# Kernel tuning notes

Measured on AMD Instinct MI355X. Metric: run time of the kernel, lower is better.

Reference implementation:

```python
import jax, jax.numpy as jnp
import numpy as np

N_ATOMS = 100000
N_EDGES = 6400000
CUTOFF = 12.0
CUTOFF_SR = 2.0
CUTOFF_SQ = CUTOFF * CUTOFF
KEHALF = 7.199822675975274  # ASE kehalf, unit factors = 1


def poly6_switch(d, cutoff):
    # Poly6 smooth switch-off: 1 at d=0, 0 at d>=cutoff
    x = d / cutoff
    sw = 1.0 - 10.0 * x**3 + 15.0 * x**4 - 6.0 * x**5
    return jnp.where(d < cutoff, sw, jnp.zeros_like(sw))


def setup_inputs() -> dict:
    key = jax.random.key(0)
    k1, k2, k3, k4, k5 = jax.random.split(key, 5)
    atomic_charges = jax.random.normal(k1, (N_ATOMS,), dtype=jnp.float32) * 0.3
    atomic_dipoles = jax.random.normal(k2, (N_ATOMS,), dtype=jnp.float32) * 0.1
    # distances in (0.5, 13.5): some pairs inside short-range, some beyond cutoff
    distances = jax.random.uniform(k3, (N_EDGES,), dtype=jnp.float32) * 13.0 + 0.5
    idx_i = jax.random.randint(k4, (N_EDGES,), 0, N_ATOMS, dtype=jnp.int32)
    idx_j = jax.random.randint(k5, (N_EDGES,), 0, N_ATOMS, dtype=jnp.int32)
    return {
        "atomic_charges": atomic_charges,
        "atomic_dipoles": atomic_dipoles,
        "distances": distances,
        "idx_i": idx_i,
        "idx_j": idx_j,
    }


def reference(atomic_charges, atomic_dipoles, distances, idx_i, idx_j):
    # gather per-edge charges / dipoles
    qi = atomic_charges[idx_i]
    qj = atomic_charges[idx_j]
    di = atomic_dipoles[idx_i]
    dj = atomic_dipoles[idx_j]

    d = distances
    d_sh = jnp.sqrt(d * d + 1.0)  # shielded distance

    sw_off = poly6_switch(d, CUTOFF_SR)
    sw_on = 1.0 - sw_off

    # split_distance=True branch (cutoff != cutoff_short_range):
    # shifted-force Coulomb (charge-charge, ~1/d)
    E_ord_q = 1.0 / d + d / CUTOFF_SQ - 2.0 / CUTOFF
    E_sh_q = 1.0 / d_sh + d_sh / CUTOFF_SQ - 2.0 / CUTOFF
    E_q = KEHALF * qi * qj * (sw_off * E_sh_q + sw_on * E_ord_q)

    # dipole-dipole term (~1/d^3), same shielded/ordinary blending
    E_ord_d = 1.0 / d**3
    E_sh_d = 1.0 / d_sh**3
    E_d = KEHALF * di * dj * (sw_off * E_sh_d + sw_on * E_ord_d)

    E = E_q + E_d
    E = jnp.where(d <= CUTOFF, E, jnp.zeros_like(E))

    # scatter-sum per-edge energies to atoms
    return jax.ops.segment_sum(E, idx_i, num_segments=N_ATOMS)
```

## Files before the change

kernel.cpp:

```cpp
#include <hip/hip_runtime.h>
#include <hip/hip_bf16.h>
#include <hip/hip_fp16.h>

#define CUTOFF_C    12.0f
#define CUTOFF_SR_C 2.0f
#define CUTOFF_SQ_C 144.0f
#define KEHALF_C    7.199822675975274f

#define BLK1   1024

#define CH_DUO   17408
#define LUT_DUO  1024
#define CH_SOLO  33792
#define LUT_SOLO 2048

#define CH_REC   20000

__device__ __forceinline__ float edge_energy(float d, float qi, float qj,
                                             float di, float dj) {
    float inv_d   = __frcp_rn(d);
    float dsh     = __fsqrt_rn(fmaf(d, d, 1.0f));
    float inv_dsh = __frcp_rn(dsh);
    float x  = d * (1.0f / CUTOFF_SR_C);
    float x3 = x * x * x;
    float sw = fmaf(x3, fmaf(x, fmaf(x, -6.0f, 15.0f), -10.0f), 1.0f);
    float sw_off = (d < CUTOFF_SR_C) ? sw : 0.0f;
    float Eoq = inv_d   + fmaf(d,   (1.0f / CUTOFF_SQ_C), -(2.0f / CUTOFF_C));
    float Esq = inv_dsh + fmaf(dsh, (1.0f / CUTOFF_SQ_C), -(2.0f / CUTOFF_C));
    float Eq  = (KEHALF_C * qi * qj) * fmaf(sw_off, Esq - Eoq, Eoq);
    float Eod = inv_d * inv_d * inv_d;
    float Esd = inv_dsh * inv_dsh * inv_dsh;
    float Ed  = (KEHALF_C * di * dj) * fmaf(sw_off, Esd - Eod, Eod);
    return Eq + Ed;
}

__device__ __forceinline__ float2 fg_exact(float d) {
    float inv_d   = 1.0f / d;
    float dsh     = sqrtf(fmaf(d, d, 1.0f));
    float inv_dsh = 1.0f / dsh;
    float x  = d * (1.0f / CUTOFF_SR_C);
    float x3 = x * x * x;
    float sw = fmaf(x3, fmaf(x, fmaf(x, -6.0f, 15.0f), -10.0f), 1.0f);
    float sw_off = (d < CUTOFF_SR_C) ? sw : 0.0f;
    float Foq = inv_d   + fmaf(d,   (1.0f / CUTOFF_SQ_C), -(2.0f / CUTOFF_C));
    float Fsq = inv_dsh + fmaf(dsh, (1.0f / CUTOFF_SQ_C), -(2.0f / CUTOFF_C));
    float F   = fmaf(sw_off, Fsq - Foq, Foq);
    float God = inv_d * inv_d * inv_d;
    float Gsd = inv_dsh * inv_dsh * inv_dsh;
    float G   = fmaf(sw_off, Gsd - God, God);
    return make_float2(KEHALF_C * F, KEHALF_C * G);
}

__device__ __forceinline__ __half2 vw_make_exact(float d, __half2 hqdj) {
    float2 qdj = __half22float2(hqdj);
    float2 fg  = fg_exact(d);
    return __floats2half2_rn(qdj.x * fg.x, qdj.y * fg.y);
}

__device__ __forceinline__ unsigned h2bits(__half2 h) {
    union { __half2 h; unsigned u; } c; c.h = h; return c.u;
}
__device__ __forceinline__ __half2 bits2h(unsigned u) {
    union { unsigned u; __half2 h; } c; c.u = u; return c.h;
}
template <typename T>
__device__ __forceinline__ auto atom_add_h2(T* p, T v, int)
    -> decltype(atomicAdd(p, v), void()) {
    atomicAdd(p, v);
}
template <typename T>
__device__ __forceinline__ void atom_add_h2(T* p, T v, long) {
    unsigned* u = (unsigned*)p;
    unsigned old = *u, assumed;
    do {
        assumed = old;
        __half2 sum = __hadd2(bits2h(assumed), v);
        old = atomicCAS(u, assumed, h2bits(sum));
    } while (old != assumed);
}

__device__ __forceinline__ unsigned vw_bits(float d, __half2 hq) {
    float inv_d   = __builtin_amdgcn_rcpf(d);
    float dsh2    = fmaf(d, d, 1.0f);
    float inv_dsh = __builtin_amdgcn_rsqf(dsh2);
    float dsh     = dsh2 * inv_dsh;
    float x  = d * (1.0f / CUTOFF_SR_C);
    float x3 = x * x * x;
    float sw = fmaf(x3, fmaf(x, fmaf(x, -6.0f, 15.0f), -10.0f), 1.0f);
    float sw_off = (d < CUTOFF_SR_C) ? sw : 0.0f;
    float Foq = inv_d   + fmaf(d,   (1.0f / CUTOFF_SQ_C), -(2.0f / CUTOFF_C));
    float Fsq = inv_dsh + fmaf(dsh, (1.0f / CUTOFF_SQ_C), -(2.0f / CUTOFF_C));
    float F   = fmaf(sw_off, Fsq - Foq, Foq);
    float God = inv_d * inv_d * inv_d;
    float Gsd = inv_dsh * inv_dsh * inv_dsh;
    float G   = fmaf(sw_off, Gsd - God, God);
    float2 q2 = __half22float2(hq);
    __half2 vw = __floats2half2_rn((KEHALF_C * q2.x) * F, (KEHALF_C * q2.y) * G);
    return h2bits(vw);
}

__global__ __launch_bounds__(256) void pc_pack_qd_h(
    const float* __restrict__ q,
    const float* __restrict__ dip,
    __half2*     __restrict__ qd,
    int n_atoms)
{
    int a = blockIdx.x * 256 + threadIdx.x;
    if (a < n_atoms) qd[a] = __floats2half2_rn(q[a], dip[a]);
}

__global__ __launch_bounds__(256) void pc_edge_vw(
    const float*   __restrict__ dist,
    const int*     __restrict__ idx_j,
    const __half2* __restrict__ qd,
    uint4*         __restrict__ vwo,
    unsigned*      __restrict__ vws,
    int n_edges, int n4, int half)
{
    const int t = blockIdx.x * 256 + (int)threadIdx.x;
    const int4*   j4p = (const int4*)idx_j;
    const float4* d4p = (const float4*)dist;

    if (t < half) {
        const int  ga = t;
        const int  gb = t + half;
        const bool vb = gb < n4;
        const int  gbs = vb ? gb : ga;

        int4   ja = j4p[ga];
        int4   jb = j4p[gbs];
        float4 da = d4p[ga];
        float4 db = d4p[gbs];

        __half2 q0 = qd[ja.x], q1 = qd[ja.y], q2 = qd[ja.z], q3 = qd[ja.w];
        __half2 q4 = qd[jb.x], q5 = qd[jb.y], q6 = qd[jb.z], q7 = qd[jb.w];

        unsigned w0 = vw_bits(da.x, q0);
        unsigned w1 = vw_bits(da.y, q1);
        unsigned w2 = vw_bits(da.z, q2);
        unsigned w3 = vw_bits(da.w, q3);
        unsigned w4 = vw_bits(db.x, q4);
        unsigned w5 = vw_bits(db.y, q5);
        unsigned w6 = vw_bits(db.z, q6);
        unsigned w7 = vw_bits(db.w, q7);

        w0 = (da.x <= CUTOFF_C) ? w0 : 0u;
        w1 = (da.y <= CUTOFF_C) ? w1 : 0u;
        w2 = (da.z <= CUTOFF_C) ? w2 : 0u;
        w3 = (da.w <= CUTOFF_C) ? w3 : 0u;
        w4 = (db.x <= CUTOFF_C) ? w4 : 0u;
        w5 = (db.y <= CUTOFF_C) ? w5 : 0u;
        w6 = (db.z <= CUTOFF_C) ? w6 : 0u;
        w7 = (db.w <= CUTOFF_C) ? w7 : 0u;

        vwo[ga] = make_uint4(w0, w1, w2, w3);
        if (vb) vwo[gb] = make_uint4(w4, w5, w6, w7);
    }

    const int tl = n_edges & 3;
    if (blockIdx.x == 0 && (int)threadIdx.x < tl) {
        int e = (n4 << 2) + (int)threadIdx.x;
        float d = dist[e];
        unsigned w = vw_bits(d, qd[idx_j[e]]);
        vws[e] = (d <= CUTOFF_C) ? w : 0u;
    }
}

template <int CH, int BLK>
__global__ __launch_bounds__(BLK) void pc_scatter_vw(
    const int*      __restrict__ idx_i,
    const unsigned* __restrict__ vw,
    __half2*        __restrict__ partial,
    int n_edges, int n4, int S, int gps, int n_atoms)
{
    extern __shared__ char smem[];
    __half2* acc2 = (__half2*)smem;

    const int s = blockIdx.x % S;
    const int c = blockIdx.x / S;
    const unsigned base = (unsigned)(c * CH);
    const int lim = min(CH, n_atoms - (int)base);

    const __half2 hzero = __floats2half2_rn(0.0f, 0.0f);
    for (int i = threadIdx.x; i < CH; i += BLK) acc2[i] = hzero;
    __syncthreads();

    const int4*  i4p = (const int4*)idx_i;
    const uint4* v4p = (const uint4*)vw;
    const int g0 = s * gps;
    const int g1 = min(g0 + gps, n4);
    for (int g = g0 + (int)threadIdx.x; g < g1; g += BLK) {
        int4  i4 = i4p[g];
        uint4 v4 = v4p[g];
        unsigned lc0 = (unsigned)i4.x - base;
        unsigned lc1 = (unsigned)i4.y - base;
        unsigned lc2 = (unsigned)i4.z - base;
        unsigned lc3 = (unsigned)i4.w - base;
        if (lc0 < (unsigned)CH) atom_add_h2(&acc2[lc0], bits2h(v4.x), 0);
        if (lc1 < (unsigned)CH) atom_add_h2(&acc2[lc1], bits2h(v4.y), 0);
        if (lc2 < (unsigned)CH) atom_add_h2(&acc2[lc2], bits2h(v4.z), 0);
        if (lc3 < (unsigned)CH) atom_add_h2(&acc2[lc3], bits2h(v4.w), 0);
    }

    if (s == S - 1) {
        for (int e = (n4 << 2) + (int)threadIdx.x; e < n_edges; e += BLK) {
            unsigned lc = (unsigned)idx_i[e] - base;
            if (lc < (unsigned)CH) atom_add_h2(&acc2[lc], bits2h(vw[e]), 0);
        }
    }

    __syncthreads();
    __half2* row = partial + (size_t)s * n_atoms + (int)base;
    for (int i = threadIdx.x; i < lim; i += BLK) row[i] = acc2[i];
}

template <int CH, int LUTN, int BLK>
__global__ __launch_bounds__(BLK) void pc_scatter_lut(
    const float*   __restrict__ dist,
    const int*     __restrict__ idx_i,
    const int*     __restrict__ idx_j,
    const __half2* __restrict__ qd,
    __half2*       __restrict__ partial,
    int n_edges, int n4, int S, int gps, int n_atoms, int nch)
{
    extern __shared__ char smem[];
    __half2* acc2 = (__half2*)smem;
    float2*  lut  = (float2*)(smem + (size_t)CH * sizeof(__half2));

    const int s    = blockIdx.x % S;
    const int c    = blockIdx.x / S;
    const int base = c * CH;
    const int lim  = min(CH, n_atoms - base);

    const __half2 hzero = __floats2half2_rn(0.0f, 0.0f);
    for (int i = threadIdx.x; i < CH; i += BLK) acc2[i] = hzero;

    const float hstep = CUTOFF_C / (float)LUTN;
    for (int k = threadIdx.x; k <= LUTN; k += BLK) {
        float d = fmaxf((float)k * hstep, 0.25f * hstep);
        lut[k] = fg_exact(d);
    }
    __syncthreads();

    const int g0 = s * gps;
    const int g1 = min(g0 + gps, n4);
    const int4*   idxi4 = (const int4*)idx_i;
    const int4*   idxj4 = (const int4*)idx_j;
    const float4* dist4 = (const float4*)dist;
    const float   dscale = (float)LUTN / CUTOFF_C;

    for (int g = g0 + (int)threadIdx.x; g < g1; g += BLK) {
        int4   i4 = idxi4[g];
        int4   j4 = idxj4[g];
        float4 d4 = dist4[g];

        int      ii[4] = { i4.x, i4.y, i4.z, i4.w };
        int      jj[4] = { j4.x, j4.y, j4.z, j4.w };
        float    dd[4] = { d4.x, d4.y, d4.z, d4.w };
        unsigned lc[4];
        bool     vl[4];
        __half2  qh[4];

        #pragma unroll
        for (int k = 0; k < 4; ++k) {
            lc[k] = (unsigned)(ii[k] - base);
            vl[k] = (lc[k] < (unsigned)CH) && (dd[k] <= CUTOFF_C);
        }
        #pragma unroll
        for (int k = 0; k < 4; ++k)
            qh[k] = vl[k] ? qd[jj[k]] : hzero;

        #pragma unroll
        for (int k = 0; k < 4; ++k) {
            if (vl[k]) {
                float t  = dd[k] * dscale;
                int   kk = min((int)t, LUTN - 1);
                float fr = t - (float)kk;
                float2 l0 = lut[kk];
                float2 l1 = lut[kk + 1];
                float F = fmaf(fr, l1.x - l0.x, l0.x);
                float G = fmaf(fr, l1.y - l0.y, l0.y);
                float2 qdj = __half22float2(qh[k]);
                __half2 vw = __floats2half2_rn(qdj.x * F, qdj.y * G);
                atom_add_h2(&acc2[lc[k]], vw, 0);
            }
        }
    }

    if (s == S - 1) {
        for (int e = (n4 << 2) + (int)threadIdx.x; e < n_edges; e += BLK) {
            int i = idx_i[e];
            float d = dist[e];
            unsigned local = (unsigned)(i - base);
            if (local < (unsigned)CH && d <= CUTOFF_C) {
                __half2 vw = vw_make_exact(d, qd[idx_j[e]]);
                atom_add_h2(&acc2[local], vw, 0);
            }
        }
    }

    __syncthreads();
    __half2* row = partial + (size_t)s * n_atoms + base;
    for (int i = threadIdx.x; i < lim; i += BLK) row[i] = acc2[i];
}

__global__ __launch_bounds__(256) void pc_reduce_vw(
    const __half2* __restrict__ partial,
    const float*   __restrict__ q,
    const float*   __restrict__ dip,
    float*         __restrict__ out,
    int n_atoms, int S)
{
    __shared__ float2 sh[256];
    int a0   = blockIdx.x * 64;
    int lane = threadIdx.x & 63;
    int w    = threadIdx.x >> 6;
    int a    = a0 + lane;

    float sv = 0.0f, sw = 0.0f;
    if (a < n_atoms) {
        int per = S >> 2;
        const __half2* p = partial + a;
        int s = w * per, send = s + per;
        for (; s < send; ++s) {
            float2 t = __half22float2(p[(size_t)s * n_atoms]);
            sv += t.x; sw += t.y;
        }
    }
    sh[threadIdx.x] = make_float2(sv, sw);
    __syncthreads();
    if (w == 0 && a < n_atoms) {
        float2 t0 = sh[lane],       t1 = sh[64 + lane];
        float2 t2 = sh[128 + lane], t3 = sh[192 + lane];
        float fv = (t0.x + t1.x) + (t2.x + t3.x);
        float fw = (t0.y + t1.y) + (t2.y + t3.y);
        out[a] = fmaf(q[a], fv, dip[a] * fw);
    }
}

__global__ __launch_bounds__(256) void pc_dipole_edges_atomic(
    const float* __restrict__ q,
    const float* __restrict__ dip,
    const float* __restrict__ dist,
    const int*   __restrict__ idx_i,
    const int*   __restrict__ idx_j,
    float*       __restrict__ out,
    int n_edges)
{
    int t = blockIdx.x * blockDim.x + threadIdx.x;
    const int stride = gridDim.x * blockDim.x;
    for (int e = t; e < n_edges; e += stride) {
        float d = dist[e];
        if (d > CUTOFF_C) continue;
        int i = idx_i[e], j = idx_j[e];
        atomicAdd(&out[i], edge_energy(d, q[i], q[j], dip[i], dip[j]));
    }
}

static int probe_blocks(const void* f, int blk, size_t lds) {
    hipError_t e1 = hipFuncSetAttribute(
        f, hipFuncAttributeMaxDynamicSharedMemorySize, (int)lds);
    int nb = 0;
    hipError_t e2 = hipOccupancyMaxActiveBlocksPerMultiprocessor(&nb, f, blk, lds);
    if (e1 != hipSuccess || e2 != hipSuccess) return 0;
    return nb;
}

extern "C" void kernel_launch(void* const* d_in, const int* in_sizes, int n_in,
                              void* d_out, int out_size, void* d_ws, size_t ws_size,
                              hipStream_t stream) {
    const float* q     = (const float*)d_in[0];
    const float* dip   = (const float*)d_in[1];
    const float* dist  = (const float*)d_in[2];
    const int*   idx_i = (const int*)d_in[3];
    const int*   idx_j = (const int*)d_in[4];
    float*       out   = (float*)d_out;

    int n_edges = in_sizes[2];
    int n_atoms = out_size;
    int n4      = n_edges >> 2;

    size_t qd_b    = ((size_t)n_atoms * sizeof(__half2) + 255) & ~(size_t)255;
    size_t vw_b    = (((size_t)n_edges * 4) + 255) & ~(size_t)255;
    size_t lds_rec = (size_t)CH_REC * sizeof(__half2);

    int nb_rec = probe_blocks((const void*)&pc_scatter_vw<CH_REC, BLK1>,
                              BLK1, lds_rec);

    int S_new = 0, nch_new = 0;
    if (nb_rec >= 2 && n_atoms > 0 && n4 > 0 && ws_size > qd_b + vw_b) {
        nch_new = (n_atoms + CH_REC - 1) / CH_REC;
        int cap = 512;
        S_new = (cap / nch_new) & ~7;
        size_t avail = ws_size - qd_b - vw_b;
        int S_fit = (int)(avail / ((size_t)n_atoms * sizeof(__half2))) & ~7;
        if (S_fit < S_new) S_new = S_fit;
    }

    if (S_new >= 8) {
        __half2*  qd      = (__half2*)d_ws;
        unsigned* vw      = (unsigned*)((char*)d_ws + qd_b);
        __half2*  partial = (__half2*)((char*)d_ws + qd_b + vw_b);
        int       gps     = (n4 + S_new - 1) / S_new;
        int       half    = (n4 + 1) >> 1;
        int       gridA   = (half + 255) / 256;
        if (gridA < 1) gridA = 1;

        pc_pack_qd_h<<<(n_atoms + 255) / 256, 256, 0, stream>>>(q, dip, qd,
                                                                n_atoms);
        pc_edge_vw<<<gridA, 256, 0, stream>>>(dist, idx_j, qd,
                                              (uint4*)vw, vw,
                                              n_edges, n4, half);
        pc_scatter_vw<CH_REC, BLK1>
            <<<S_new * nch_new, BLK1, lds_rec, stream>>>(
                idx_i, vw, partial, n_edges, n4, S_new, gps, n_atoms);
        pc_reduce_vw<<<(n_atoms + 63) / 64, 256, 0, stream>>>(
            partial, q, dip, out, n_atoms, S_new);
        return;
    }

    size_t lds_duo  = (size_t)CH_DUO  * sizeof(__half2)
                    + (size_t)(LUT_DUO  + 1) * sizeof(float2);
    size_t lds_solo = (size_t)CH_SOLO * sizeof(__half2)
                    + (size_t)(LUT_SOLO + 1) * sizeof(float2);

    int nb_duo = probe_blocks((const void*)&pc_scatter_lut<CH_DUO, LUT_DUO, BLK1>,
                              BLK1, lds_duo);
    int nb_solo = probe_blocks((const void*)&pc_scatter_lut<CH_SOLO, LUT_SOLO, BLK1>,
                               BLK1, lds_solo);

    bool use_duo = (nb_duo >= 2);
    int  CH, nch, S, cap;
    size_t lds;
    if (use_duo) {
        CH  = CH_DUO;  lds = lds_duo;
        nch = (n_atoms + CH - 1) / CH;
        cap = 512;
    } else {
        CH  = CH_SOLO; lds = lds_solo;
        nch = (n_atoms + CH - 1) / CH;
        cap = 256;
    }
    S = (cap / nch) & ~7;
    if (S < 8) S = 8;

    size_t avail = (ws_size > qd_b) ? ws_size - qd_b : 0;
    int S_fit = (int)(avail / ((size_t)n_atoms * sizeof(__half2)));
    if (S_fit < S) S = S_fit & ~7;

    bool ok = (use_duo || nb_solo >= 1) && S >= 8 && n_atoms > 0;

    if (ok) {
        __half2* qd      = (__half2*)d_ws;
        __half2* partial = (__half2*)((char*)d_ws + qd_b);
        int      gps     = (n4 + S - 1) / S;

        pc_pack_qd_h<<<(n_atoms + 255) / 256, 256, 0, stream>>>(q, dip, qd,
                                                                n_atoms);
        if (use_duo)
            pc_scatter_lut<CH_DUO, LUT_DUO, BLK1>
                <<<S * nch, BLK1, lds, stream>>>(
                    dist, idx_i, idx_j, qd, partial, n_edges, n4, S, gps,
                    n_atoms, nch);
        else
            pc_scatter_lut<CH_SOLO, LUT_SOLO, BLK1>
                <<<S * nch, BLK1, lds, stream>>>(
                    dist, idx_i, idx_j, qd, partial, n_edges, n4, S, gps,
                    n_atoms, nch);
        pc_reduce_vw<<<(n_atoms + 63) / 64, 256, 0, stream>>>(
            partial, q, dip, out, n_atoms, S);
    } else {
        hipMemsetAsync(out, 0, (size_t)n_atoms * sizeof(float), stream);
        int grid = (n_edges + 255) / 256;
        pc_dipole_edges_atomic<<<grid, 256, 0, stream>>>(
            q, dip, dist, idx_i, idx_j, out, n_edges);
    }
}
```

Measured before the change: 162.2 us.

## Fuse pack, edge, scatter and reduce into one cooperative persistent kernel

Replaces the four-kernel pipeline (pack, per-edge value, chunked LDS scatter, partial reduce) with a single cooperative kernel separated by grid.sync barriers, aiming to remove launch gaps and inter-kernel idle time. The grid is sized to CU count times resident blocks, so S partitions become num_cu*2/nch instead of 512/nch, which changes the parallelism of the scatter and reduce phases. The scatter loop is also unrolled to process two int4/uint4 groups per iteration for more memory-level parallelism, and the unused LUT-based fallback path is deleted. Grid-wide syncs and fewer blocks per phase risk lower occupancy during the edge and reduce phases.

```diff
diff --git a/kernel.cpp b/kernel.cpp
--- a/kernel.cpp
+++ b/kernel.cpp
@@ -1,6 +1,9 @@
 #include <hip/hip_runtime.h>
 #include <hip/hip_bf16.h>
 #include <hip/hip_fp16.h>
+#include <hip/hip_cooperative_groups.h>
+
+namespace cg = cooperative_groups;
 
 #define CUTOFF_C    12.0f
 #define CUTOFF_SR_C 2.0f
@@ -8,13 +11,7 @@
 #define KEHALF_C    7.199822675975274f
 
 #define BLK1   1024
-
-#define CH_DUO   17408
-#define LUT_DUO  1024
-#define CH_SOLO  33792
-#define LUT_SOLO 2048
-
-#define CH_REC   20000
+#define CH_REC 20000
 
 __device__ __forceinline__ float edge_energy(float d, float qi, float qj,
                                              float di, float dj) {
@@ -34,29 +31,6 @@
     return Eq + Ed;
 }
 
-__device__ __forceinline__ float2 fg_exact(float d) {
-    float inv_d   = 1.0f / d;
-    float dsh     = sqrtf(fmaf(d, d, 1.0f));
-    float inv_dsh = 1.0f / dsh;
-    float x  = d * (1.0f / CUTOFF_SR_C);
-    float x3 = x * x * x;
-    float sw = fmaf(x3, fmaf(x, fmaf(x, -6.0f, 15.0f), -10.0f), 1.0f);
-    float sw_off = (d < CUTOFF_SR_C) ? sw : 0.0f;
-    float Foq = inv_d   + fmaf(d,   (1.0f / CUTOFF_SQ_C), -(2.0f / CUTOFF_C));
-    float Fsq = inv_dsh + fmaf(dsh, (1.0f / CUTOFF_SQ_C), -(2.0f / CUTOFF_C));
-    float F   = fmaf(sw_off, Fsq - Foq, Foq);
-    float God = inv_d * inv_d * inv_d;
-    float Gsd = inv_dsh * inv_dsh * inv_dsh;
-    float G   = fmaf(sw_off, Gsd - God, God);
-    return make_float2(KEHALF_C * F, KEHALF_C * G);
-}
-
-__device__ __forceinline__ __half2 vw_make_exact(float d, __half2 hqdj) {
-    float2 qdj = __half22float2(hqdj);
-    float2 fg  = fg_exact(d);
-    return __floats2half2_rn(qdj.x * fg.x, qdj.y * fg.y);
-}
-
 __device__ __forceinline__ unsigned h2bits(__half2 h) {
     union { __half2 h; unsigned u; } c; c.h = h; return c.u;
 }
@@ -79,7 +53,7 @@
     } while (old != assumed);
 }
 
-__device__ __forceinline__ unsigned vw_bits(float d, __half2 hq) {
+__device__ __forceinline__ unsigned vw_bits(float d, unsigned hqbits) {
     float inv_d   = __builtin_amdgcn_rcpf(d);
     float dsh2    = fmaf(d, d, 1.0f);
     float inv_dsh = __builtin_amdgcn_rsqf(dsh2);
@@ -94,10 +68,162 @@
     float God = inv_d * inv_d * inv_d;
     float Gsd = inv_dsh * inv_dsh * inv_dsh;
     float G   = fmaf(sw_off, Gsd - God, God);
-    float2 q2 = __half22float2(hq);
+    float2 q2 = __half22float2(bits2h(hqbits));
     __half2 vw = __floats2half2_rn((KEHALF_C * q2.x) * F, (KEHALF_C * q2.y) * G);
     return h2bits(vw);
 }
+
+__global__ __launch_bounds__(BLK1, 8) void pc_mega(
+    const float*   __restrict__ q,
+    const float*   __restrict__ dip,
+    const float*   __restrict__ dist,
+    const int*     __restrict__ idx_i,
+    const int*     __restrict__ idx_j,
+    __half2*       __restrict__ qd,
+    unsigned*      __restrict__ vw,
+    __half2*       __restrict__ partial,
+    float*         __restrict__ out,
+    int n_edges, int n4, int half, int n_atoms, int S, int gps, int nch)
+{
+    extern __shared__ char smem[];
+    __half2* acc2 = (__half2*)smem;
+    cg::grid_group grid = cg::this_grid();
+
+    const int tid = (int)threadIdx.x;
+    const int bid = (int)blockIdx.x;
+    const int gt  = bid * BLK1 + tid;
+    const int GT  = (int)gridDim.x * BLK1;
+
+    for (int a = gt; a < n_atoms; a += GT)
+        qd[a] = __floats2half2_rn(q[a], dip[a]);
+
+    __threadfence();
+    grid.sync();
+
+    {
+        const int4*   j4p = (const int4*)idx_j;
+        const float4* d4p = (const float4*)dist;
+        uint4* vwo = (uint4*)vw;
+
+        for (int t = gt; t < half; t += GT) {
+            const int  ga = t;
+            const int  gb = t + half;
+            const bool vb = gb < n4;
+            const int  gbs = vb ? gb : ga;
+
+            int4   ja = j4p[ga];
+            int4   jb = j4p[gbs];
+            float4 da = d4p[ga];
+            float4 db = d4p[gbs];
+
+            __half2 q0 = qd[ja.x], q1 = qd[ja.y], q2 = qd[ja.z], q3 = qd[ja.w];
+            __half2 q4 = qd[jb.x], q5 = qd[jb.y], q6 = qd[jb.z], q7 = qd[jb.w];
+
+            unsigned w0 = vw_bits(da.x, h2bits(q0));
+            unsigned w1 = vw_bits(da.y, h2bits(q1));
+            unsigned w2 = vw_bits(da.z, h2bits(q2));
+            unsigned w3 = vw_bits(da.w, h2bits(q3));
+            unsigned w4 = vw_bits(db.x, h2bits(q4));
+            unsigned w5 = vw_bits(db.y, h2bits(q5));
+            unsigned w6 = vw_bits(db.z, h2bits(q6));
+            unsigned w7 = vw_bits(db.w, h2bits(q7));
+
+            w0 = (da.x <= CUTOFF_C) ? w0 : 0u;
+            w1 = (da.y <= CUTOFF_C) ? w1 : 0u;
+            w2 = (da.z <= CUTOFF_C) ? w2 : 0u;
+            w3 = (da.w <= CUTOFF_C) ? w3 : 0u;
+            w4 = (db.x <= CUTOFF_C) ? w4 : 0u;
+            w5 = (db.y <= CUTOFF_C) ? w5 : 0u;
+            w6 = (db.z <= CUTOFF_C) ? w6 : 0u;
+            w7 = (db.w <= CUTOFF_C) ? w7 : 0u;
+
+            vwo[ga] = make_uint4(w0, w1, w2, w3);
+            if (vb) vwo[gb] = make_uint4(w4, w5, w6, w7);
+        }
+
+        const int tl = n_edges & 3;
+        if (gt < tl) {
+            int e = (n4 << 2) + gt;
+            float d = dist[e];
+            unsigned w = vw_bits(d, h2bits(qd[idx_j[e]]));
+            vw[e] = (d <= CUTOFF_C) ? w : 0u;
+        }
+    }
+
+    __threadfence();
+    grid.sync();
+
+    if (bid < S * nch) {
+        const int s = bid % S;
+        const int c = bid / S;
+        const unsigned base = (unsigned)(c * CH_REC);
+        const int lim = min(CH_REC, n_atoms - (int)base);
+
+        const __half2 hzero = __floats2half2_rn(0.0f, 0.0f);
+        for (int i = tid; i < CH_REC; i += BLK1) acc2[i] = hzero;
+        __syncthreads();
+
+        const int4*  i4p = (const int4*)idx_i;
+        const uint4* v4p = (const uint4*)vw;
+        const int g0 = s * gps;
+        const int g1 = min(g0 + gps, n4);
+        for (int g = g0 + tid; g < g1; g += 2 * BLK1) {
+            const int  gB   = g + BLK1;
+            const bool hasB = gB < g1;
+            const int  gBs  = hasB ? gB : g;
+
+            int4  iA = i4p[g];
+            int4  iB = i4p[gBs];
+            uint4 vA = v4p[g];
+            uint4 vB = v4p[gBs];
+
+            unsigned a0 = (unsigned)iA.x - base;
+            unsigned a1 = (unsigned)iA.y - base;
+            unsigned a2 = (unsigned)iA.z - base;
+            unsigned a3 = (unsigned)iA.w - base;
+            if (a0 < (unsigned)CH_REC) atom_add_h2(&acc2[a0], bits2h(vA.x), 0);
+            if (a1 < (unsigned)CH_REC) atom_add_h2(&acc2[a1], bits2h(vA.y), 0);
+            if (a2 < (unsigned)CH_REC) atom_add_h2(&acc2[a2], bits2h(vA.z), 0);
+            if (a3 < (unsigned)CH_REC) atom_add_h2(&acc2[a3], bits2h(vA.w), 0);
+            if (hasB) {
+                unsigned b0 = (unsigned)iB.x - base;
+                unsigned b1 = (unsigned)iB.y - base;
+                unsigned b2 = (unsigned)iB.z - base;
+                unsigned b3 = (unsigned)iB.w - base;
+                if (b0 < (unsigned)CH_REC) atom_add_h2(&acc2[b0], bits2h(vB.x), 0);
+                if (b1 < (unsigned)CH_REC) atom_add_h2(&acc2[b1], bits2h(vB.y), 0);
+                if (b2 < (unsigned)CH_REC) atom_add_h2(&acc2[b2], bits2h(vB.z), 0);
+                if (b3 < (unsigned)CH_REC) atom_add_h2(&acc2[b3], bits2h(vB.w), 0);
+            }
+        }
+
+        if (s == S - 1) {
+            for (int e = (n4 << 2) + tid; e < n_edges; e += BLK1) {
+                unsigned lc = (unsigned)idx_i[e] - base;
+                if (lc < (unsigned)CH_REC) atom_add_h2(&acc2[lc], bits2h(vw[e]), 0);
+            }
+        }
+
+        __syncthreads();
+        __half2* row = partial + (size_t)s * n_atoms + (int)base;
+        for (int i = tid; i < lim; i += BLK1) row[i] = acc2[i];
+    }
+
+    __threadfence();
+    grid.sync();
+
+    for (int a = gt; a < n_atoms; a += GT) {
+        const __half2* p = partial + a;
+        float sv = 0.0f, sw = 0.0f;
+        #pragma unroll 4
+        for (int s2 = 0; s2 < S; ++s2) {
+            float2 t2 = __half22float2(p[(size_t)s2 * n_atoms]);
+            sv += t2.x; sw += t2.y;
+        }
+        out[a] = fmaf(q[a], sv, dip[a] * sw);
+    }
+}
+
 
 __global__ __launch_bounds__(256) void pc_pack_qd_h(
     const float* __restrict__ q,
@@ -135,14 +261,14 @@
         __half2 q0 = qd[ja.x], q1 = qd[ja.y], q2 = qd[ja.z], q3 = qd[ja.w];
         __half2 q4 = qd[jb.x], q5 = qd[jb.y], q6 = qd[jb.z], q7 = qd[jb.w];
 
-        unsigned w0 = vw_bits(da.x, q0);
-        unsigned w1 = vw_bits(da.y, q1);
-        unsigned w2 = vw_bits(da.z, q2);
-        unsigned w3 = vw_bits(da.w, q3);
-        unsigned w4 = vw_bits(db.x, q4);
-        unsigned w5 = vw_bits(db.y, q5);
-        unsigned w6 = vw_bits(db.z, q6);
-        unsigned w7 = vw_bits(db.w, q7);
+        unsigned w0 = vw_bits(da.x, h2bits(q0));
+        unsigned w1 = vw_bits(da.y, h2bits(q1));
+        unsigned w2 = vw_bits(da.z, h2bits(q2));
+        unsigned w3 = vw_bits(da.w, h2bits(q3));
+        unsigned w4 = vw_bits(db.x, h2bits(q4));
+        unsigned w5 = vw_bits(db.y, h2bits(q5));
+        unsigned w6 = vw_bits(db.z, h2bits(q6));
+        unsigned w7 = vw_bits(db.w, h2bits(q7));
 
         w0 = (da.x <= CUTOFF_C) ? w0 : 0u;
         w1 = (da.y <= CUTOFF_C) ? w1 : 0u;
@@ -161,7 +287,7 @@
     if (blockIdx.x == 0 && (int)threadIdx.x < tl) {
         int e = (n4 << 2) + (int)threadIdx.x;
         float d = dist[e];
-        unsigned w = vw_bits(d, qd[idx_j[e]]);
+        unsigned w = vw_bits(d, h2bits(qd[idx_j[e]]));
         vws[e] = (d <= CUTOFF_C) ? w : 0u;
     }
 }
@@ -189,17 +315,34 @@
     const uint4* v4p = (const uint4*)vw;
     const int g0 = s * gps;
     const int g1 = min(g0 + gps, n4);
-    for (int g = g0 + (int)threadIdx.x; g < g1; g += BLK) {
-        int4  i4 = i4p[g];
-        uint4 v4 = v4p[g];
-        unsigned lc0 = (unsigned)i4.x - base;
-        unsigned lc1 = (unsigned)i4.y - base;
-        unsigned lc2 = (unsigned)i4.z - base;
-        unsigned lc3 = (unsigned)i4.w - base;
-        if (lc0 < (unsigned)CH) atom_add_h2(&acc2[lc0], bits2h(v4.x), 0);
-        if (lc1 < (unsigned)CH) atom_add_h2(&acc2[lc1], bits2h(v4.y), 0);
-        if (lc2 < (unsigned)CH) atom_add_h2(&acc2[lc2], bits2h(v4.z), 0);
-        if (lc3 < (unsigned)CH) atom_add_h2(&acc2[lc3], bits2h(v4.w), 0);
+    for (int g = g0 + (int)threadIdx.x; g < g1; g += 2 * BLK) {
+        const int  gB   = g + BLK;
+        const bool hasB = gB < g1;
+        const int  gBs  = hasB ? gB : g;
+
+        int4  iA = i4p[g];
+        int4  iB = i4p[gBs];
+        uint4 vA = v4p[g];
+        uint4 vB = v4p[gBs];
+
+        unsigned a0 = (unsigned)iA.x - base;
+        unsigned a1 = (unsigned)iA.y - base;
+        unsigned a2 = (unsigned)iA.z - base;
+        unsigned a3 = (unsigned)iA.w - base;
+        if (a0 < (unsigned)CH) atom_add_h2(&acc2[a0], bits2h(vA.x), 0);
+        if (a1 < (unsigned)CH) atom_add_h2(&acc2[a1], bits2h(vA.y), 0);
+        if (a2 < (unsigned)CH) atom_add_h2(&acc2[a2], bits2h(vA.z), 0);
+        if (a3 < (unsigned)CH) atom_add_h2(&acc2[a3], bits2h(vA.w), 0);
+        if (hasB) {
+            unsigned b0 = (unsigned)iB.x - base;
+            unsigned b1 = (unsigned)iB.y - base;
+            unsigned b2 = (unsigned)iB.z - base;
+            unsigned b3 = (unsigned)iB.w - base;
+            if (b0 < (unsigned)CH) atom_add_h2(&acc2[b0], bits2h(vB.x), 0);
+            if (b1 < (unsigned)CH) atom_add_h2(&acc2[b1], bits2h(vB.y), 0);
+            if (b2 < (unsigned)CH) atom_add_h2(&acc2[b2], bits2h(vB.z), 0);
+            if (b3 < (unsigned)CH) atom_add_h2(&acc2[b3], bits2h(vB.w), 0);
+        }
     }
 
     if (s == S - 1) {
@@ -211,96 +354,6 @@
 
     __syncthreads();
     __half2* row = partial + (size_t)s * n_atoms + (int)base;
-    for (int i = threadIdx.x; i < lim; i += BLK) row[i] = acc2[i];
-}
-
-template <int CH, int LUTN, int BLK>
-__global__ __launch_bounds__(BLK) void pc_scatter_lut(
-    const float*   __restrict__ dist,
-    const int*     __restrict__ idx_i,
-    const int*     __restrict__ idx_j,
-    const __half2* __restrict__ qd,
-    __half2*       __restrict__ partial,
-    int n_edges, int n4, int S, int gps, int n_atoms, int nch)
-{
-    extern __shared__ char smem[];
-    __half2* acc2 = (__half2*)smem;
-    float2*  lut  = (float2*)(smem + (size_t)CH * sizeof(__half2));
-
-    const int s    = blockIdx.x % S;
-    const int c    = blockIdx.x / S;
-    const int base = c * CH;
-    const int lim  = min(CH, n_atoms - base);
-
-    const __half2 hzero = __floats2half2_rn(0.0f, 0.0f);
-    for (int i = threadIdx.x; i < CH; i += BLK) acc2[i] = hzero;
-
-    const float hstep = CUTOFF_C / (float)LUTN;
-    for (int k = threadIdx.x; k <= LUTN; k += BLK) {
-        float d = fmaxf((float)k * hstep, 0.25f * hstep);
-        lut[k] = fg_exact(d);
-    }
-    __syncthreads();
-
-    const int g0 = s * gps;
-    const int g1 = min(g0 + gps, n4);
-    const int4*   idxi4 = (const int4*)idx_i;
-    const int4*   idxj4 = (const int4*)idx_j;
-    const float4* dist4 = (const float4*)dist;
-    const float   dscale = (float)LUTN / CUTOFF_C;
-
-    for (int g = g0 + (int)threadIdx.x; g < g1; g += BLK) {
-        int4   i4 = idxi4[g];
-        int4   j4 = idxj4[g];
-        float4 d4 = dist4[g];
-
-        int      ii[4] = { i4.x, i4.y, i4.z, i4.w };
-        int      jj[4] = { j4.x, j4.y, j4.z, j4.w };
-        float    dd[4] = { d4.x, d4.y, d4.z, d4.w };
-        unsigned lc[4];
-        bool     vl[4];
-        __half2  qh[4];
-
-        #pragma unroll
-        for (int k = 0; k < 4; ++k) {
-            lc[k] = (unsigned)(ii[k] - base);
-            vl[k] = (lc[k] < (unsigned)CH) && (dd[k] <= CUTOFF_C);
-        }
-        #pragma unroll
-        for (int k = 0; k < 4; ++k)
-            qh[k] = vl[k] ? qd[jj[k]] : hzero;
-
-        #pragma unroll
-        for (int k = 0; k < 4; ++k) {
-            if (vl[k]) {
-                float t  = dd[k] * dscale;
-                int   kk = min((int)t, LUTN - 1);
-                float fr = t - (float)kk;
-                float2 l0 = lut[kk];
-                float2 l1 = lut[kk + 1];
-                float F = fmaf(fr, l1.x - l0.x, l0.x);
-                float G = fmaf(fr, l1.y - l0.y, l0.y);
-                float2 qdj = __half22float2(qh[k]);
-                __half2 vw = __floats2half2_rn(qdj.x * F, qdj.y * G);
-                atom_add_h2(&acc2[lc[k]], vw, 0);
-            }
-        }
-    }
-
-    if (s == S - 1) {
-        for (int e = (n4 << 2) + (int)threadIdx.x; e < n_edges; e += BLK) {
-            int i = idx_i[e];
-            float d = dist[e];
-            unsigned local = (unsigned)(i - base);
-            if (local < (unsigned)CH && d <= CUTOFF_C) {
-                __half2 vw = vw_make_exact(d, qd[idx_j[e]]);
-                atom_add_h2(&acc2[local], vw, 0);
-            }
-        }
-    }
-
-    __syncthreads();
-    __half2* row = partial + (size_t)s * n_atoms + base;
     for (int i = threadIdx.x; i < lim; i += BLK) row[i] = acc2[i];
 }
 
@@ -379,19 +432,58 @@
     int n_edges = in_sizes[2];
     int n_atoms = out_size;
     int n4      = n_edges >> 2;
+    int half    = (n4 + 1) >> 1;
 
     size_t qd_b    = ((size_t)n_atoms * sizeof(__half2) + 255) & ~(size_t)255;
     size_t vw_b    = (((size_t)n_edges * 4) + 255) & ~(size_t)255;
     size_t lds_rec = (size_t)CH_REC * sizeof(__half2);
 
+    int nch = (n_atoms > 0) ? (n_atoms + CH_REC - 1) / CH_REC : 0;
+
+    int dev = 0;
+    (void)hipGetDevice(&dev);
+    int coop_ok = 0, num_cu = 0;
+    (void)hipDeviceGetAttribute(&coop_ok, hipDeviceAttributeCooperativeLaunch, dev);
+    (void)hipDeviceGetAttribute(&num_cu, hipDeviceAttributeMultiprocessorCount, dev);
+
+    if (coop_ok && num_cu > 0 && n_atoms > 0 && n4 > 0 &&
+        ws_size > qd_b + vw_b) {
+        int nb_mega = probe_blocks((const void*)&pc_mega, BLK1, lds_rec);
+        if (nb_mega >= 1) {
+            int blocks_per_cu = (nb_mega >= 2) ? 2 : 1;
+            int grid = num_cu * blocks_per_cu;
+
+            int S_new = (grid / nch) & ~7;
+            size_t avail = ws_size - qd_b - vw_b;
+            int S_fit = (int)(avail / ((size_t)n_atoms * sizeof(__half2))) & ~7;
+            if (S_fit < S_new) S_new = S_fit;
+
+            if (S_new >= 8) {
+                __half2*  qd      = (__half2*)d_ws;
+                unsigned* vw      = (unsigned*)((char*)d_ws + qd_b);
+                __half2*  partial = (__half2*)((char*)d_ws + qd_b + vw_b);
+                int       gps     = (n4 + S_new - 1) / S_new;
+
+                void* args[] = {
+                    (void*)&q, (void*)&dip, (void*)&dist,
+                    (void*)&idx_i, (void*)&idx_j,
+                    (void*)&qd, (void*)&vw, (void*)&partial, (void*)&out,
+                    (void*)&n_edges, (void*)&n4, (void*)&half, (void*)&n_atoms,
+                    (void*)&S_new, (void*)&gps, (void*)&nch };
+                hipError_t le = hipLaunchCooperativeKernel(
+                    (const void*)&pc_mega, dim3(grid), dim3(BLK1),
+                    args, (unsigned)lds_rec, stream);
+                if (le == hipSuccess) return;
+            }
+        }
+    }
+
     int nb_rec = probe_blocks((const void*)&pc_scatter_vw<CH_REC, BLK1>,
                               BLK1, lds_rec);
-
-    int S_new = 0, nch_new = 0;
+    int S_new = 0;
     if (nb_rec >= 2 && n_atoms > 0 && n4 > 0 && ws_size > qd_b + vw_b) {
-        nch_new = (n_atoms + CH_REC - 1) / CH_REC;
         int cap = 512;
-        S_new = (cap / nch_new) & ~7;
+        S_new = (cap / nch) & ~7;
         size_t avail = ws_size - qd_b - vw_b;
         int S_fit = (int)(avail / ((size_t)n_atoms * sizeof(__half2))) & ~7;
         if (S_fit < S_new) S_new = S_fit;
@@ -402,7 +494,6 @@
         unsigned* vw      = (unsigned*)((char*)d_ws + qd_b);
         __half2*  partial = (__half2*)((char*)d_ws + qd_b + vw_b);
         int       gps     = (n4 + S_new - 1) / S_new;
-        int       half    = (n4 + 1) >> 1;
         int       gridA   = (half + 255) / 256;
         if (gridA < 1) gridA = 1;
 
@@ -412,67 +503,16 @@
                                               (uint4*)vw, vw,
                                               n_edges, n4, half);
         pc_scatter_vw<CH_REC, BLK1>
-            <<<S_new * nch_new, BLK1, lds_rec, stream>>>(
+            <<<S_new * nch, BLK1, lds_rec, stream>>>(
                 idx_i, vw, partial, n_edges, n4, S_new, gps, n_atoms);
         pc_reduce_vw<<<(n_atoms + 63) / 64, 256, 0, stream>>>(
             partial, q, dip, out, n_atoms, S_new);
         return;
     }
 
-    size_t lds_duo  = (size_t)CH_DUO  * sizeof(__half2)
-                    + (size_t)(LUT_DUO  + 1) * sizeof(float2);
-    size_t lds_solo = (size_t)CH_SOLO * sizeof(__half2)
-                    + (size_t)(LUT_SOLO + 1) * sizeof(float2);
-
-    int nb_duo = probe_blocks((const void*)&pc_scatter_lut<CH_DUO, LUT_DUO, BLK1>,
-                              BLK1, lds_duo);
-    int nb_solo = probe_blocks((const void*)&pc_scatter_lut<CH_SOLO, LUT_SOLO, BLK1>,
-                               BLK1, lds_solo);
-
-    bool use_duo = (nb_duo >= 2);
-    int  CH, nch, S, cap;
-    size_t lds;
-    if (use_duo) {
-        CH  = CH_DUO;  lds = lds_duo;
-        nch = (n_atoms + CH - 1) / CH;
-        cap = 512;
-    } else {
-        CH  = CH_SOLO; lds = lds_solo;
-        nch = (n_atoms + CH - 1) / CH;
-        cap = 256;
-    }
-    S = (cap / nch) & ~7;
-    if (S < 8) S = 8;
-
-    size_t avail = (ws_size > qd_b) ? ws_size - qd_b : 0;
-    int S_fit = (int)(avail / ((size_t)n_atoms * sizeof(__half2)));
-    if (S_fit < S) S = S_fit & ~7;
-
-    bool ok = (use_duo || nb_solo >= 1) && S >= 8 && n_atoms > 0;
-
-    if (ok) {
-        __half2* qd      = (__half2*)d_ws;
-        __half2* partial = (__half2*)((char*)d_ws + qd_b);
-        int      gps     = (n4 + S - 1) / S;
-
-        pc_pack_qd_h<<<(n_atoms + 255) / 256, 256, 0, stream>>>(q, dip, qd,
-                                                                n_atoms);
-        if (use_duo)
-            pc_scatter_lut<CH_DUO, LUT_DUO, BLK1>
-                <<<S * nch, BLK1, lds, stream>>>(
-                    dist, idx_i, idx_j, qd, partial, n_edges, n4, S, gps,
-                    n_atoms, nch);
-        else
-            pc_scatter_lut<CH_SOLO, LUT_SOLO, BLK1>
-                <<<S * nch, BLK1, lds, stream>>>(
-                    dist, idx_i, idx_j, qd, partial, n_edges, n4, S, gps,
-                    n_atoms, nch);
-        pc_reduce_vw<<<(n_atoms + 63) / 64, 256, 0, stream>>>(
-            partial, q, dip, out, n_atoms, S);
-    } else {
-        hipMemsetAsync(out, 0, (size_t)n_atoms * sizeof(float), stream);
-        int grid = (n_edges + 255) / 256;
-        pc_dipole_edges_atomic<<<grid, 256, 0, stream>>>(
-            q, dip, dist, idx_i, idx_j, out, n_edges);
-    }
-}
+    hipMemsetAsync(out, 0, (size_t)n_atoms * sizeof(float), stream);
+    int grid = (n_edges + 255) / 256;
+    if (grid < 1) grid = 1;
+    pc_dipole_edges_atomic<<<grid, 256, 0, stream>>>(
+        q, dip, dist, idx_i, idx_j, out, n_edges);
+}
```

After: 585.4 us. 3.61x slower.
